# Kernel tuning notes

Measured on AMD Instinct MI355X. Metric: run time of the kernel, lower is better.

The kernel has to match this reference:

```python
import jax, jax.numpy as jnp
import numpy as np

B, T, E, U, V = 4096, 80, 100, 64, 10000

def setup_inputs() -> dict:
    key = jax.random.key(0)
    ks = jax.random.split(key, 10)
    s = lambda *sh: 0.05
    return {
        "tokens": jax.random.randint(ks[0], (B, T), 0, V, dtype=jnp.int32),
        "emb": jax.random.normal(ks[1], (V, E), jnp.float32) * 0.05,
        "k0": jax.random.normal(ks[2], (E, 4 * U), jnp.float32) * 0.05,
        "r0": jax.random.normal(ks[3], (U, 4 * U), jnp.float32) * 0.05,
        "b0": jnp.zeros((4 * U,), jnp.float32),
        "k1": jax.random.normal(ks[4], (E, 4 * U), jnp.float32) * 0.05,
        "r1": jax.random.normal(ks[5], (U, 4 * U), jnp.float32) * 0.05,
        "b1": jnp.zeros((4 * U,), jnp.float32),
        "Wd": jax.random.normal(ks[6], (U, 1), jnp.float32) * 0.05,
        "bd": jnp.zeros((1,), jnp.float32),
    }

def _lstm_cell(h, c, xt, k, r, b):
    # keras LSTMCell gate order: i, f, g(cell candidate), o
    z = xt @ k + h @ r + b  # [B, 4U]
    i, f, g, o = jnp.split(z, 4, axis=-1)
    c_new = jax.nn.sigmoid(f) * c + jax.nn.sigmoid(i) * jnp.tanh(g)
    h_new = jax.nn.sigmoid(o) * jnp.tanh(c_new)
    return h_new, c_new

def reference(tokens, emb, k0, r0, b0, k1, r1, b1, Wd, bd):
    x = emb[tokens]                 # [B, T, E]
    xs = jnp.swapaxes(x, 0, 1)      # [T, B, E] for scan over time
    zeros = jnp.zeros((tokens.shape[0], U), x.dtype)
    init = (zeros, zeros, zeros, zeros)  # h0, c0, h1, c1

    def step(state, xt):
        h0, c0, h1, c1 = state
        h0, c0 = _lstm_cell(h0, c0, xt, k0, r0, b0)
        # NOTE: original feeds the raw embedded word (not out0) to cell 1
        h1, c1 = _lstm_cell(h1, c1, xt, k1, r1, b1)
        return (h0, c0, h1, c1), None

    (h0, c0, h1, c1), _ = jax.lax.scan(step, init, xs)
    logits = h1 @ Wd + bd           # [B, 1]
    return jax.nn.sigmoid(logits)
```

## Files before the change

### kernel.cpp

```cpp
#include <hip/hip_runtime.h>
#include <hip/hip_bf16.h>
#include <stdint.h>

#define B_  4096
#define T_  80
#define E_  100
#define U_  64
#define G_  256
#define V_  10000

#define S_H  72
#define AS   136
#define KS2  132
#define TS   81
#define XS   260

typedef __attribute__((ext_vector_type(8))) __bf16 bf16x8;
typedef __attribute__((ext_vector_type(4))) __bf16 bf16x4;
typedef __attribute__((ext_vector_type(4))) float  floatx4;

__device__ __forceinline__ float sigmoidf_(float x) {
    return __builtin_amdgcn_rcpf(1.f + __expf(-x));
}

__device__ __forceinline__ float tanhf_(float x) {
    return fmaf(-2.f, __builtin_amdgcn_rcpf(__expf(2.f * x) + 1.f), 1.f);
}

__device__ __forceinline__ void gload16(const float* gsrc, const float* ldst) {
    __builtin_amdgcn_global_load_lds(
        (const __attribute__((address_space(1))) void*)(uintptr_t)gsrc,
        (__attribute__((address_space(3))) void*)(uintptr_t)ldst,
        16, 0, 0);
}

__global__ __launch_bounds__(256) void embk_kernel(const float* __restrict__ emb,
                                                   const float* __restrict__ k1,
                                                   const float* __restrict__ b1,
                                                   float* __restrict__ embk) {
    __shared__ __bf16 aLDS[64 * AS];
    __shared__ __bf16 kLDS[128 * KS2];

    const int tid  = threadIdx.x;
    const int lane = tid & 63;
    const int w    = tid >> 6;
    const int n    = lane & 15;
    const int kg   = lane >> 4;
    const int v0   = (blockIdx.x >> 1) * 64;
    const int n0   = (blockIdx.x & 1) * 128;
    const int nrows = min(64, V_ - v0);

    for (int i = tid; i < 64 * AS / 8; i += 256) {
        bf16x8 z;
#pragma unroll
        for (int jj = 0; jj < 8; ++jj) z[jj] = (__bf16)0.f;
        *(bf16x8*)(aLDS + i * 8) = z;
    }
    for (int i = tid; i < 28 * KS2; i += 256)
        kLDS[100 * KS2 + i] = (__bf16)0.f;

    const float bv0 = b1[n0 + w * 32 + n];
    const float bv1 = b1[n0 + w * 32 + 16 + n];

    __syncthreads();

    for (int i = tid; i < nrows * 25; i += 256) {
        int r = i / 25, q = i - r * 25;
        float4 ev = *(const float4*)(emb + (long)(v0 + r) * E_ + q * 4);
        bf16x4 bv; bv[0] = (__bf16)ev.x; bv[1] = (__bf16)ev.y;
                   bv[2] = (__bf16)ev.z; bv[3] = (__bf16)ev.w;
        *(bf16x4*)(aLDS + r * AS + q * 4) = bv;
    }
    for (int i = tid; i < 100 * 32; i += 256) {
        int k = i >> 5, cq = (i & 31) * 4;
        float4 kv = *(const float4*)(k1 + (long)k * G_ + n0 + cq);
        bf16x4 bv; bv[0] = (__bf16)kv.x; bv[1] = (__bf16)kv.y;
                   bv[2] = (__bf16)kv.z; bv[3] = (__bf16)kv.w;
        *(bf16x4*)(kLDS + k * KS2 + cq) = bv;
    }
    __syncthreads();

    bf16x8 bfr[2][4];
#pragma unroll
    for (int ct = 0; ct < 2; ++ct)
#pragma unroll
        for (int kc = 0; kc < 4; ++kc) {
            bf16x8 s;
#pragma unroll
            for (int jj = 0; jj < 8; ++jj)
                s[jj] = kLDS[(kc * 32 + kg * 8 + jj) * KS2 + w * 32 + ct * 16 + n];
            bfr[ct][kc] = s;
        }

#pragma unroll
    for (int mt = 0; mt < 4; ++mt) {
        const __bf16* ab = aLDS + (mt * 16 + n) * AS + kg * 8;
        bf16x8 a0 = *(const bf16x8*)(ab + 0);
        bf16x8 a1 = *(const bf16x8*)(ab + 32);
        bf16x8 a2 = *(const bf16x8*)(ab + 64);
        bf16x8 a3 = *(const bf16x8*)(ab + 96);
#pragma unroll
        for (int ct = 0; ct < 2; ++ct) {
            float bv = ct ? bv1 : bv0;
            floatx4 acc = {bv, bv, bv, bv};
            acc = __builtin_amdgcn_mfma_f32_16x16x32_bf16(a0, bfr[ct][0], acc, 0, 0, 0);
            acc = __builtin_amdgcn_mfma_f32_16x16x32_bf16(a1, bfr[ct][1], acc, 0, 0, 0);
            acc = __builtin_amdgcn_mfma_f32_16x16x32_bf16(a2, bfr[ct][2], acc, 0, 0, 0);
            acc = __builtin_amdgcn_mfma_f32_16x16x32_bf16(a3, bfr[ct][3], acc, 0, 0, 0);
#pragma unroll
            for (int r = 0; r < 4; ++r) {
                int v = v0 + mt * 16 + kg * 4 + r;
                if (v < V_) embk[(long)v * G_ + n0 + w * 32 + ct * 16 + n] = acc[r];
            }
        }
    }
}

template<int SEL, int RB, int WB>
__device__ __forceinline__ void lstm_step(
        int tt, int n, int kg, int w, int lane,
        const int* __restrict__ tokLDS,
        __bf16 (&hbuf)[2][16 * S_H],
        float (&xstage)[3][16 * XS],
        const bf16x8 (&afr)[4][2],
        const float* __restrict__ embk,
        float (&c)[4]) {
    const __bf16* hb = &hbuf[SEL ^ 1][0];
    bf16x8 hb0 = *(const bf16x8*)(hb + n * S_H + kg * 8);
    bf16x8 hb1 = *(const bf16x8*)(hb + n * S_H + 32 + kg * 8);
    const float* xrow = &xstage[RB][0] + n * XS + w * 16 + kg * 4;
    floatx4 a0 = *(const floatx4*)(xrow + 0);
    floatx4 a1 = *(const floatx4*)(xrow + 64);
    floatx4 a2 = *(const floatx4*)(xrow + 128);
    floatx4 a3 = *(const floatx4*)(xrow + 192);

#pragma unroll
    for (int j = 0; j < 4; ++j) {
        int tok = __builtin_amdgcn_readfirstlane(tokLDS[(w * 4 + j) * TS + tt]);
        gload16(embk + (long)tok * G_ + (lane << 2),
                &xstage[WB][0] + (w * 4 + j) * XS);
    }

    a0 = __builtin_amdgcn_mfma_f32_16x16x32_bf16(afr[0][0], hb0, a0, 0, 0, 0);
    a0 = __builtin_amdgcn_mfma_f32_16x16x32_bf16(afr[0][1], hb1, a0, 0, 0, 0);
    a1 = __builtin_amdgcn_mfma_f32_16x16x32_bf16(afr[1][0], hb0, a1, 0, 0, 0);
    a1 = __builtin_amdgcn_mfma_f32_16x16x32_bf16(afr[1][1], hb1, a1, 0, 0, 0);
    a2 = __builtin_amdgcn_mfma_f32_16x16x32_bf16(afr[2][0], hb0, a2, 0, 0, 0);
    a2 = __builtin_amdgcn_mfma_f32_16x16x32_bf16(afr[2][1], hb1, a2, 0, 0, 0);
    a3 = __builtin_amdgcn_mfma_f32_16x16x32_bf16(afr[3][0], hb0, a3, 0, 0, 0);
    a3 = __builtin_amdgcn_mfma_f32_16x16x32_bf16(afr[3][1], hb1, a3, 0, 0, 0);

    bf16x4 hv;
#pragma unroll
    for (int r = 0; r < 4; ++r) {
        float zi = a0[r], zf = a1[r], zg = a2[r], zo = a3[r];
        float cn = fmaf(sigmoidf_(zf), c[r], sigmoidf_(zi) * tanhf_(zg));
        float hn = sigmoidf_(zo) * tanhf_(cn);
        c[r] = cn;
        hv[r] = (__bf16)hn;
    }
    *(bf16x4*)(&hbuf[SEL][0] + n * S_H + w * 16 + kg * 4) = hv;

    asm volatile("s_waitcnt lgkmcnt(0) vmcnt(4)\n\ts_barrier" ::: "memory");
}

__global__ __launch_bounds__(256) void lstm_kernel(const int*   __restrict__ tokens,
                                                   const float* __restrict__ embk,
                                                   const float* __restrict__ r1,
                                                   const float* __restrict__ Wd,
                                                   const float* __restrict__ bd,
                                                   float* __restrict__ out) {
    __shared__ int    tokLDS[16 * TS];
    __shared__ __bf16 hbuf[2][16 * S_H];
    __shared__ float  xstage[3][16 * XS];

    const int tid  = threadIdx.x;
    const int lane = tid & 63;
    const int w    = tid >> 6;
    const int n    = lane & 15;
    const int kg   = lane >> 4;
    const int bb   = blockIdx.x * 16;

    for (int i = tid; i < 16 * T_; i += 256)
        tokLDS[(i / T_) * TS + (i % T_)] = tokens[bb * T_ + i];
    for (int i = tid; i < 2 * 16 * S_H; i += 256) (&hbuf[0][0])[i] = (__bf16)0.f;

    bf16x8 afr[4][2];
#pragma unroll
    for (int ct = 0; ct < 4; ++ct)
#pragma unroll
        for (int kc = 0; kc < 2; ++kc) {
            bf16x8 s;
#pragma unroll
            for (int jj = 0; jj < 8; ++jj)
                s[jj] = (__bf16)r1[(kc * 32 + kg * 8 + jj) * G_ + ct * 64 + w * 16 + n];
            afr[ct][kc] = s;
        }

    float c[4] = {0.f, 0.f, 0.f, 0.f};

    __syncthreads();

#pragma unroll
    for (int s = 0; s < 2; ++s)
#pragma unroll
        for (int j = 0; j < 4; ++j) {
            int tok = __builtin_amdgcn_readfirstlane(tokLDS[(w * 4 + j) * TS + s]);
            gload16(embk + (long)tok * G_ + (lane << 2),
                    &xstage[s][0] + (w * 4 + j) * XS);
        }
    asm volatile("s_waitcnt lgkmcnt(0) vmcnt(4)\n\ts_barrier" ::: "memory");

    for (int t = 0; t < 78; t += 6) {
        lstm_step<0, 0, 2>(t + 2, n, kg, w, lane, tokLDS, hbuf, xstage, afr, embk, c);
        lstm_step<1, 1, 0>(t + 3, n, kg, w, lane, tokLDS, hbuf, xstage, afr, embk, c);
        lstm_step<0, 2, 1>(t + 4, n, kg, w, lane, tokLDS, hbuf, xstage, afr, embk, c);
        lstm_step<1, 0, 2>(t + 5, n, kg, w, lane, tokLDS, hbuf, xstage, afr, embk, c);
        lstm_step<0, 1, 0>(t + 6, n, kg, w, lane, tokLDS, hbuf, xstage, afr, embk, c);
        lstm_step<1, 2, 1>(t + 7, n, kg, w, lane, tokLDS, hbuf, xstage, afr, embk, c);
    }
    lstm_step<0, 0, 2>(79, n, kg, w, lane, tokLDS, hbuf, xstage, afr, embk, c);
    lstm_step<1, 1, 0>(79, n, kg, w, lane, tokLDS, hbuf, xstage, afr, embk, c);

    asm volatile("s_waitcnt vmcnt(0)" ::: "memory");

    if (tid < 16) {
        const __bf16* hb = hbuf[1] + tid * S_H;
        float s = bd[0];
#pragma unroll
        for (int u = 0; u < U_; ++u) s = fmaf((float)hb[u], Wd[u], s);
        out[bb + tid] = sigmoidf_(s);
    }
}

extern "C" void kernel_launch(void* const* d_in, const int* in_sizes, int n_in,
                              void* d_out, int out_size, void* d_ws, size_t ws_size,
                              hipStream_t stream) {
    const int*   tokens = (const int*)  d_in[0];
    const float* emb    = (const float*)d_in[1];
    const float* k1     = (const float*)d_in[5];
    const float* r1     = (const float*)d_in[6];
    const float* b1     = (const float*)d_in[7];
    const float* Wd     = (const float*)d_in[8];
    const float* bd     = (const float*)d_in[9];
    float*       out    = (float*)d_out;

    float* embk = (float*)d_ws;

    embk_kernel<<<((V_ + 63) / 64) * 2, 256, 0, stream>>>(emb, k1, b1, embk);
    lstm_kernel<<<B_ / 16, 256, 0, stream>>>(tokens, embk, r1, Wd, bd, out);
}
```

Before: 137.9 us.

## Halve LSTM block to two waves, each computing 32 hidden units

Reduces the recurrent LSTM kernel from 256 to 128 threads per block. Each wave now holds two 16-column tiles per gate, double the recurrent weight fragments and cell state, and issues eight embedding row gathers per step instead of four. This cuts per-step barrier participants and wave count, but doubles serial MFMA and transcendental work per wave on the latency-bound recurrence. It also drops readfirstlane on token indices.

```diff
diff --git a/kernel.cpp b/kernel.cpp
--- a/kernel.cpp
+++ b/kernel.cpp
@@ -33,6 +33,8 @@
         (__attribute__((address_space(3))) void*)(uintptr_t)ldst,
         16, 0, 0);
 }
+
+#define MFMA16(A,B,C) __builtin_amdgcn_mfma_f32_16x16x32_bf16(A, B, C, 0, 0, 0)
 
 __global__ __launch_bounds__(256) void embk_kernel(const float* __restrict__ emb,
                                                    const float* __restrict__ k1,
@@ -103,10 +105,10 @@
         for (int ct = 0; ct < 2; ++ct) {
             float bv = ct ? bv1 : bv0;
             floatx4 acc = {bv, bv, bv, bv};
-            acc = __builtin_amdgcn_mfma_f32_16x16x32_bf16(a0, bfr[ct][0], acc, 0, 0, 0);
-            acc = __builtin_amdgcn_mfma_f32_16x16x32_bf16(a1, bfr[ct][1], acc, 0, 0, 0);
-            acc = __builtin_amdgcn_mfma_f32_16x16x32_bf16(a2, bfr[ct][2], acc, 0, 0, 0);
-            acc = __builtin_amdgcn_mfma_f32_16x16x32_bf16(a3, bfr[ct][3], acc, 0, 0, 0);
+            acc = MFMA16(a0, bfr[ct][0], acc);
+            acc = MFMA16(a1, bfr[ct][1], acc);
+            acc = MFMA16(a2, bfr[ct][2], acc);
+            acc = MFMA16(a3, bfr[ct][3], acc);
 #pragma unroll
             for (int r = 0; r < 4; ++r) {
                 int v = v0 + mt * 16 + kg * 4 + r;
@@ -122,49 +124,54 @@
         const int* __restrict__ tokLDS,
         __bf16 (&hbuf)[2][16 * S_H],
         float (&xstage)[3][16 * XS],
-        const bf16x8 (&afr)[4][2],
+        const bf16x8 (&afr)[4][2][2],
         const float* __restrict__ embk,
-        float (&c)[4]) {
+        float (&c)[8]) {
     const __bf16* hb = &hbuf[SEL ^ 1][0];
     bf16x8 hb0 = *(const bf16x8*)(hb + n * S_H + kg * 8);
     bf16x8 hb1 = *(const bf16x8*)(hb + n * S_H + 32 + kg * 8);
-    const float* xrow = &xstage[RB][0] + n * XS + w * 16 + kg * 4;
-    floatx4 a0 = *(const floatx4*)(xrow + 0);
-    floatx4 a1 = *(const floatx4*)(xrow + 64);
-    floatx4 a2 = *(const floatx4*)(xrow + 128);
-    floatx4 a3 = *(const floatx4*)(xrow + 192);
-
-#pragma unroll
-    for (int j = 0; j < 4; ++j) {
-        int tok = __builtin_amdgcn_readfirstlane(tokLDS[(w * 4 + j) * TS + tt]);
+    const float* xrow = &xstage[RB][0] + n * XS + w * 32 + kg * 4;
+    floatx4 acc[4][2];
+#pragma unroll
+    for (int g = 0; g < 4; ++g)
+#pragma unroll
+        for (int c2 = 0; c2 < 2; ++c2)
+            acc[g][c2] = *(const floatx4*)(xrow + g * 64 + c2 * 16);
+
+#pragma unroll
+    for (int j = 0; j < 8; ++j) {
+        int tok = tokLDS[(w * 8 + j) * TS + tt];
         gload16(embk + (long)tok * G_ + (lane << 2),
-                &xstage[WB][0] + (w * 4 + j) * XS);
-    }
-
-    a0 = __builtin_amdgcn_mfma_f32_16x16x32_bf16(afr[0][0], hb0, a0, 0, 0, 0);
-    a0 = __builtin_amdgcn_mfma_f32_16x16x32_bf16(afr[0][1], hb1, a0, 0, 0, 0);
-    a1 = __builtin_amdgcn_mfma_f32_16x16x32_bf16(afr[1][0], hb0, a1, 0, 0, 0);
-    a1 = __builtin_amdgcn_mfma_f32_16x16x32_bf16(afr[1][1], hb1, a1, 0, 0, 0);
-    a2 = __builtin_amdgcn_mfma_f32_16x16x32_bf16(afr[2][0], hb0, a2, 0, 0, 0);
-    a2 = __builtin_amdgcn_mfma_f32_16x16x32_bf16(afr[2][1], hb1, a2, 0, 0, 0);
-    a3 = __builtin_amdgcn_mfma_f32_16x16x32_bf16(afr[3][0], hb0, a3, 0, 0, 0);
-    a3 = __builtin_amdgcn_mfma_f32_16x16x32_bf16(afr[3][1], hb1, a3, 0, 0, 0);
-
-    bf16x4 hv;
-#pragma unroll
-    for (int r = 0; r < 4; ++r) {
-        float zi = a0[r], zf = a1[r], zg = a2[r], zo = a3[r];
-        float cn = fmaf(sigmoidf_(zf), c[r], sigmoidf_(zi) * tanhf_(zg));
-        float hn = sigmoidf_(zo) * tanhf_(cn);
-        c[r] = cn;
-        hv[r] = (__bf16)hn;
-    }
-    *(bf16x4*)(&hbuf[SEL][0] + n * S_H + w * 16 + kg * 4) = hv;
-
-    asm volatile("s_waitcnt lgkmcnt(0) vmcnt(4)\n\ts_barrier" ::: "memory");
-}
-
-__global__ __launch_bounds__(256) void lstm_kernel(const int*   __restrict__ tokens,
+                &xstage[WB][0] + (w * 8 + j) * XS);
+    }
+
+#pragma unroll
+    for (int g = 0; g < 4; ++g)
+#pragma unroll
+        for (int c2 = 0; c2 < 2; ++c2) {
+            acc[g][c2] = MFMA16(afr[g][c2][0], hb0, acc[g][c2]);
+            acc[g][c2] = MFMA16(afr[g][c2][1], hb1, acc[g][c2]);
+        }
+
+#pragma unroll
+    for (int c2 = 0; c2 < 2; ++c2) {
+        bf16x4 hv;
+#pragma unroll
+        for (int r = 0; r < 4; ++r) {
+            float zi = acc[0][c2][r], zf = acc[1][c2][r];
+            float zg = acc[2][c2][r], zo = acc[3][c2][r];
+            float cn = fmaf(sigmoidf_(zf), c[c2 * 4 + r], sigmoidf_(zi) * tanhf_(zg));
+            float hn = sigmoidf_(zo) * tanhf_(cn);
+            c[c2 * 4 + r] = cn;
+            hv[r] = (__bf16)hn;
+        }
+        *(bf16x4*)(&hbuf[SEL][0] + n * S_H + w * 32 + c2 * 16 + kg * 4) = hv;
+    }
+
+    asm volatile("s_waitcnt lgkmcnt(0) vmcnt(8)\n\ts_barrier" ::: "memory");
+}
+
+__global__ __launch_bounds__(128) void lstm_kernel(const int*   __restrict__ tokens,
                                                    const float* __restrict__ embk,
                                                    const float* __restrict__ r1,
                                                    const float* __restrict__ Wd,
@@ -181,35 +188,38 @@
     const int kg   = lane >> 4;
     const int bb   = blockIdx.x * 16;
 
-    for (int i = tid; i < 16 * T_; i += 256)
+    for (int i = tid; i < 16 * T_; i += 128)
         tokLDS[(i / T_) * TS + (i % T_)] = tokens[bb * T_ + i];
-    for (int i = tid; i < 2 * 16 * S_H; i += 256) (&hbuf[0][0])[i] = (__bf16)0.f;
-
-    bf16x8 afr[4][2];
-#pragma unroll
-    for (int ct = 0; ct < 4; ++ct)
-#pragma unroll
-        for (int kc = 0; kc < 2; ++kc) {
-            bf16x8 s;
-#pragma unroll
-            for (int jj = 0; jj < 8; ++jj)
-                s[jj] = (__bf16)r1[(kc * 32 + kg * 8 + jj) * G_ + ct * 64 + w * 16 + n];
-            afr[ct][kc] = s;
-        }
-
-    float c[4] = {0.f, 0.f, 0.f, 0.f};
+    for (int i = tid; i < 2 * 16 * S_H; i += 128) (&hbuf[0][0])[i] = (__bf16)0.f;
+
+    bf16x8 afr[4][2][2];
+#pragma unroll
+    for (int g = 0; g < 4; ++g)
+#pragma unroll
+        for (int c2 = 0; c2 < 2; ++c2)
+#pragma unroll
+            for (int kc = 0; kc < 2; ++kc) {
+                bf16x8 s;
+#pragma unroll
+                for (int jj = 0; jj < 8; ++jj)
+                    s[jj] = (__bf16)r1[(kc * 32 + kg * 8 + jj) * G_
+                                       + g * 64 + w * 32 + c2 * 16 + n];
+                afr[g][c2][kc] = s;
+            }
+
+    float c[8] = {0.f, 0.f, 0.f, 0.f, 0.f, 0.f, 0.f, 0.f};
 
     __syncthreads();
 
 #pragma unroll
     for (int s = 0; s < 2; ++s)
 #pragma unroll
-        for (int j = 0; j < 4; ++j) {
-            int tok = __builtin_amdgcn_readfirstlane(tokLDS[(w * 4 + j) * TS + s]);
+        for (int j = 0; j < 8; ++j) {
+            int tok = tokLDS[(w * 8 + j) * TS + s];
             gload16(embk + (long)tok * G_ + (lane << 2),
-                    &xstage[s][0] + (w * 4 + j) * XS);
-        }
-    asm volatile("s_waitcnt lgkmcnt(0) vmcnt(4)\n\ts_barrier" ::: "memory");
+                    &xstage[s][0] + (w * 8 + j) * XS);
+        }
+    asm volatile("s_waitcnt lgkmcnt(0) vmcnt(8)\n\ts_barrier" ::: "memory");
 
     for (int t = 0; t < 78; t += 6) {
         lstm_step<0, 0, 2>(t + 2, n, kg, w, lane, tokLDS, hbuf, xstage, afr, embk, c);
@@ -248,5 +258,5 @@
     float* embk = (float*)d_ws;
 
     embk_kernel<<<((V_ + 63) / 64) * 2, 256, 0, stream>>>(emb, k1, b1, embk);
-    lstm_kernel<<<B_ / 16, 256, 0, stream>>>(tokens, embk, r1, Wd, bd, out);
-}
+    lstm_kernel<<<B_ / 16, 128, 0, stream>>>(tokens, embk, r1, Wd, bd, out);
+}
```

After: 168.8 us. 22.4% more time.
